# Kernel tuning notes

Hardware: AMD Instinct MI355X
Metric: run time of the kernel (lower is better)

The kernel has to match this reference:

```python
import jax, jax.numpy as jnp
import numpy as np

ALPHA = 2.0   # snntorch ATan surrogate default
THRESH = 1.0  # snntorch Leaky default threshold

@jax.custom_vjp
def spike(x):
    return (x > 0).astype(x.dtype)

def _spike_fwd(x):
    return spike(x), x

def _spike_bwd(x, g):
    # ATan surrogate gradient: (alpha/2) / (1 + (pi/2 * alpha * x)^2)
    return (g * (ALPHA / 2) / (1 + (jnp.pi / 2 * ALPHA * x) ** 2),)

spike.defvjp(_spike_fwd, _spike_bwd)

def _lif(inp, mem, beta):
    # snntorch Leaky, reset_mechanism='subtract':
    # reset from previous mem (detached), then integrate, then fire
    reset = jax.lax.stop_gradient(spike(mem - THRESH))
    mem = jnp.clip(beta, 0.0, 1.0) * mem + inp - reset * THRESH
    spk = spike(mem - THRESH)
    return spk, mem

def setup_inputs() -> dict:
    key = jax.random.key(0)
    ks = jax.random.split(key, 8)
    V, H, T, B = 32000, 512, 512, 8
    s = 0.02
    inv = 1.0 / np.sqrt(H)
    return {
        "x": jax.random.randint(ks[0], (T, B), 0, V),
        "emb": jax.random.normal(ks[1], (V, H), jnp.float32) * s,
        "pos_emb": jax.random.normal(ks[2], (T, H), jnp.float32) * s,
        "beta1": jnp.full((H,), 0.9, jnp.float32),
        "beta2": jnp.full((H,), 0.9, jnp.float32),
        "beta3": jnp.full((H,), 0.9, jnp.float32),
        "W2": jax.random.normal(ks[3], (H, H), jnp.float32) * inv,
        "b2": jnp.zeros((H,), jnp.float32),
        "W3": jax.random.normal(ks[4], (H, H), jnp.float32) * inv,
        "b3": jnp.zeros((H,), jnp.float32),
        "Wout": jax.random.normal(ks[5], (V, H), jnp.float32) * inv,
        "bout": jnp.zeros((V,), jnp.float32),
    }

def reference(x, emb, pos_emb, beta1, beta2, beta3, W2, b2, W3, b3, Wout, bout):
    T, B = x.shape
    H = emb.shape[1]
    # precompute token + positional embedding for all steps: [T, B, H]
    hid = emb[x] + pos_emb[:, None, :]
    mem0 = jnp.zeros((B, H), emb.dtype)

    def step(carry, h_t):
        m1, m2, m3 = carry
        spk1, m1 = _lif(h_t, m1, beta1)
        h = jax.nn.relu(spk1 @ W2.T + b2)
        spk2, m2 = _lif(h, m2, beta2)
        h = jax.nn.relu(spk2 @ W3.T + b3)
        spk3, m3 = _lif(h, m3, beta3)
        logits = spk3 @ Wout.T + bout  # [B, V]
        return (m1, m2, m3), logits

    _, out = jax.lax.scan(step, (mem0, mem0, mem0), hid)
    return out  # [T, B, V]
```

## Files before the change

kernel.cpp:

```cpp
#include <hip/hip_runtime.h>

#define TT 512
#define BB 8
#define HH 512
#define VV 32000
#define RR (TT * BB)

__device__ __forceinline__ float clip01(float x) { return fminf(fmaxf(x, 0.0f), 1.0f); }

__global__ void __launch_bounds__(512) snn_scan_kernel(
        const int* __restrict__ x, const float* __restrict__ emb,
        const float* __restrict__ pos,
        const float* __restrict__ beta1, const float* __restrict__ beta2,
        const float* __restrict__ beta3,
        const float* __restrict__ W2, const float* __restrict__ b2,
        const float* __restrict__ W3, const float* __restrict__ b3,
        int* __restrict__ act1, int* __restrict__ act2, int* __restrict__ act3,
        int* __restrict__ cnt3_g) {
    __shared__ int x_lds[TT];
    __shared__ int c1[TT], c2[TT], c3[TT];
    const int b = blockIdx.x;
    const int h = threadIdx.x;

    x_lds[h] = x[h * BB + b];
    c1[h] = 0; c2[h] = 0; c3[h] = 0;
    __syncthreads();

    {
        float bt = clip01(beta1[h]);
        float m = 0.0f;
        for (int t0 = 0; t0 < TT; t0 += 32) {
            float ev[32], pv[32];
#pragma unroll
            for (int u = 0; u < 32; ++u) {
                int xv = x_lds[t0 + u];
                ev[u] = emb[((size_t)xv << 9) + h];
                pv[u] = pos[((t0 + u) << 9) + h];
            }
#pragma unroll
            for (int u = 0; u < 32; ++u) {
                float inp = ev[u] + pv[u];
                float reset = (m > 1.0f) ? 1.0f : 0.0f;
                m = bt * m + inp - reset;
                if (m > 1.0f) {
                    int t = t0 + u;
                    int p = atomicAdd(&c1[t], 1);
                    act1[((t * BB + b) << 9) + p] = h;
                }
            }
        }
    }
    __syncthreads();

    {
        float bh = b2[h];
        float inp0 = fmaxf(bh, 0.0f);
        float bt = clip01(beta2[h]);
        float m = 0.0f;
        for (int t0 = 0; t0 < TT; t0 += 16) {
            int n[16];
#pragma unroll
            for (int u = 0; u < 16; ++u) n[u] = c1[t0 + u];
#pragma unroll
            for (int u = 0; u < 16; ++u) {
                float inp;
                if (n[u] == 0) {
                    inp = inp0;
                } else {
                    float acc = bh;
                    const int* a = act1 + (((t0 + u) * BB + b) << 9);
                    for (int i = 0; i < n[u]; ++i) acc += W2[(h << 9) + a[i]];
                    inp = fmaxf(acc, 0.0f);
                }
                float reset = (m > 1.0f) ? 1.0f : 0.0f;
                m = bt * m + inp - reset;
                if (m > 1.0f) {
                    int t = t0 + u;
                    int p = atomicAdd(&c2[t], 1);
                    act2[((t * BB + b) << 9) + p] = h;
                }
            }
        }
    }
    __syncthreads();

    {
        float bh = b3[h];
        float inp0 = fmaxf(bh, 0.0f);
        float bt = clip01(beta3[h]);
        float m = 0.0f;
        for (int t0 = 0; t0 < TT; t0 += 16) {
            int n[16];
#pragma unroll
            for (int u = 0; u < 16; ++u) n[u] = c2[t0 + u];
#pragma unroll
            for (int u = 0; u < 16; ++u) {
                float inp;
                if (n[u] == 0) {
                    inp = inp0;
                } else {
                    float acc = bh;
                    const int* a = act2 + (((t0 + u) * BB + b) << 9);
                    for (int i = 0; i < n[u]; ++i) acc += W3[(h << 9) + a[i]];
                    inp = fmaxf(acc, 0.0f);
                }
                float reset = (m > 1.0f) ? 1.0f : 0.0f;
                m = bt * m + inp - reset;
                if (m > 1.0f) {
                    int t = t0 + u;
                    int p = atomicAdd(&c3[t], 1);
                    act3[((t * BB + b) << 9) + p] = h;
                }
            }
        }
    }
    __syncthreads();
    cnt3_g[h * BB + b] = c3[h];
}

#define ROWS_PER_BLK 8

__global__ void __launch_bounds__(512) out_gemm_kernel(
        const int* __restrict__ cnt, const int* __restrict__ act,
        const float* __restrict__ Wout, const float* __restrict__ bout,
        float* __restrict__ out) {
    const int tid = threadIdx.x;
    const int v0 = tid * 4;

    float4 bv[16];
#pragma unroll
    for (int k = 0; k < 16; ++k) {
        int v = v0 + k * 2048;
        if (v < VV) bv[k] = *(const float4*)(bout + v);
    }

    const int r0 = blockIdx.x * ROWS_PER_BLK;
#pragma unroll
    for (int rr = 0; rr < ROWS_PER_BLK; ++rr) {
        const int r = r0 + rr;
        const int n = cnt[r];
        float* __restrict__ orow = out + (size_t)r * VV;
        if (n == 0) {
#pragma unroll
            for (int k = 0; k < 16; ++k) {
                int v = v0 + k * 2048;
                if (v < VV) *(float4*)(orow + v) = bv[k];
            }
        } else {
            const int* __restrict__ a = act + (r << 9);
#pragma unroll
            for (int k = 0; k < 16; ++k) {
                int v = v0 + k * 2048;
                if (v < VV) {
                    float4 acc = bv[k];
                    for (int i = 0; i < n; ++i) {
                        int kk = a[i];
                        acc.x += Wout[(size_t)(v + 0) * HH + kk];
                        acc.y += Wout[(size_t)(v + 1) * HH + kk];
                        acc.z += Wout[(size_t)(v + 2) * HH + kk];
                        acc.w += Wout[(size_t)(v + 3) * HH + kk];
                    }
                    *(float4*)(orow + v) = acc;
                }
            }
        }
    }
}

extern "C" void kernel_launch(void* const* d_in, const int* in_sizes, int n_in,
                              void* d_out, int out_size, void* d_ws, size_t ws_size,
                              hipStream_t stream) {
    const int*   x     = (const int*)d_in[0];
    const float* emb   = (const float*)d_in[1];
    const float* pos   = (const float*)d_in[2];
    const float* beta1 = (const float*)d_in[3];
    const float* beta2 = (const float*)d_in[4];
    const float* beta3 = (const float*)d_in[5];
    const float* W2    = (const float*)d_in[6];
    const float* b2    = (const float*)d_in[7];
    const float* W3    = (const float*)d_in[8];
    const float* b3    = (const float*)d_in[9];
    const float* Wout  = (const float*)d_in[10];
    const float* bout  = (const float*)d_in[11];
    float* out = (float*)d_out;

    int* act1 = (int*)d_ws;
    int* act2 = act1 + (size_t)RR * HH;
    int* act3 = act2 + (size_t)RR * HH;
    int* cnt3 = act3 + (size_t)RR * HH;

    snn_scan_kernel<<<BB, HH, 0, stream>>>(x, emb, pos, beta1, beta2, beta3,
                                           W2, b2, W3, b3, act1, act2, act3, cnt3);
    out_gemm_kernel<<<RR / ROWS_PER_BLK, HH, 0, stream>>>(cnt3, act3, Wout, bout, out);
}
```

Measured before the change: 687.0 us.

## Overlap bias broadcast of output rows with the serial scan kernel

Extra blocks are added to the scan launch. They write the bias vector into every output row while the eight scan blocks run the serial LIF recurrence. The second kernel becomes a fixup that leaves early when all its rows have zero spikes, and only computes sparse logits for rows that fired. This hides the 524 MB output write behind the latency-bound scan. The cost is that rows with spikes get written twice, and the extra blocks compete with the scan blocks for bandwidth.

Result: slower. 711.8 us (+3.6%).

```diff
diff --git a/kernel.cpp b/kernel.cpp
--- a/kernel.cpp
+++ b/kernel.cpp
@@ -6,9 +6,13 @@
 #define VV 32000
 #define RR (TT * BB)
 
+#define SCAN_BLOCKS  8
+#define BCAST_ROWS   8
+#define BCAST_BLOCKS (RR / BCAST_ROWS)
+
 __device__ __forceinline__ float clip01(float x) { return fminf(fmaxf(x, 0.0f), 1.0f); }
 
-__global__ void __launch_bounds__(512) snn_scan_kernel(
+__global__ void __launch_bounds__(512) scan_bcast_kernel(
         const int* __restrict__ x, const float* __restrict__ emb,
         const float* __restrict__ pos,
         const float* __restrict__ beta1, const float* __restrict__ beta2,
@@ -16,7 +20,31 @@
         const float* __restrict__ W2, const float* __restrict__ b2,
         const float* __restrict__ W3, const float* __restrict__ b3,
         int* __restrict__ act1, int* __restrict__ act2, int* __restrict__ act3,
-        int* __restrict__ cnt3_g) {
+        int* __restrict__ cnt3_g,
+        const float* __restrict__ bout, float* __restrict__ out) {
+
+    if (blockIdx.x >= SCAN_BLOCKS) {
+        const int tid = threadIdx.x;
+        const int v0 = tid * 4;
+        float4 bv[16];
+#pragma unroll
+        for (int k = 0; k < 16; ++k) {
+            int v = v0 + k * 2048;
+            if (v < VV) bv[k] = *(const float4*)(bout + v);
+        }
+        const int r0 = (blockIdx.x - SCAN_BLOCKS) * BCAST_ROWS;
+#pragma unroll
+        for (int rr = 0; rr < BCAST_ROWS; ++rr) {
+            float* __restrict__ orow = out + (size_t)(r0 + rr) * VV;
+#pragma unroll
+            for (int k = 0; k < 16; ++k) {
+                int v = v0 + k * 2048;
+                if (v < VV) *(float4*)(orow + v) = bv[k];
+            }
+        }
+        return;
+    }
+
     __shared__ int x_lds[TT];
     __shared__ int c1[TT], c2[TT], c3[TT];
     const int b = blockIdx.x;
@@ -118,50 +146,40 @@
     cnt3_g[h * BB + b] = c3[h];
 }
 
-#define ROWS_PER_BLK 8
-
-__global__ void __launch_bounds__(512) out_gemm_kernel(
+__global__ void __launch_bounds__(512) fixup_kernel(
         const int* __restrict__ cnt, const int* __restrict__ act,
         const float* __restrict__ Wout, const float* __restrict__ bout,
         float* __restrict__ out) {
+    __shared__ int ns[BCAST_ROWS];
+    const int r0 = blockIdx.x * BCAST_ROWS;
+    if (threadIdx.x < BCAST_ROWS) ns[threadIdx.x] = cnt[r0 + threadIdx.x];
+    __syncthreads();
+    int any = 0;
+#pragma unroll
+    for (int i = 0; i < BCAST_ROWS; ++i) any |= ns[i];
+    if (any == 0) return;
+
     const int tid = threadIdx.x;
     const int v0 = tid * 4;
-
-    float4 bv[16];
-#pragma unroll
-    for (int k = 0; k < 16; ++k) {
-        int v = v0 + k * 2048;
-        if (v < VV) bv[k] = *(const float4*)(bout + v);
-    }
-
-    const int r0 = blockIdx.x * ROWS_PER_BLK;
-#pragma unroll
-    for (int rr = 0; rr < ROWS_PER_BLK; ++rr) {
+    for (int rr = 0; rr < BCAST_ROWS; ++rr) {
+        const int n = ns[rr];
+        if (n == 0) continue;
         const int r = r0 + rr;
-        const int n = cnt[r];
+        const int* __restrict__ a = act + (r << 9);
         float* __restrict__ orow = out + (size_t)r * VV;
-        if (n == 0) {
-#pragma unroll
-            for (int k = 0; k < 16; ++k) {
-                int v = v0 + k * 2048;
-                if (v < VV) *(float4*)(orow + v) = bv[k];
-            }
-        } else {
-            const int* __restrict__ a = act + (r << 9);
-#pragma unroll
-            for (int k = 0; k < 16; ++k) {
-                int v = v0 + k * 2048;
-                if (v < VV) {
-                    float4 acc = bv[k];
-                    for (int i = 0; i < n; ++i) {
-                        int kk = a[i];
-                        acc.x += Wout[(size_t)(v + 0) * HH + kk];
-                        acc.y += Wout[(size_t)(v + 1) * HH + kk];
-                        acc.z += Wout[(size_t)(v + 2) * HH + kk];
-                        acc.w += Wout[(size_t)(v + 3) * HH + kk];
-                    }
-                    *(float4*)(orow + v) = acc;
-                }
+#pragma unroll
+        for (int k = 0; k < 16; ++k) {
+            int v = v0 + k * 2048;
+            if (v < VV) {
+                float4 acc = *(const float4*)(bout + v);
+                for (int i = 0; i < n; ++i) {
+                    int kk = a[i];
+                    acc.x += Wout[(size_t)(v + 0) * HH + kk];
+                    acc.y += Wout[(size_t)(v + 1) * HH + kk];
+                    acc.z += Wout[(size_t)(v + 2) * HH + kk];
+                    acc.w += Wout[(size_t)(v + 3) * HH + kk];
+                }
+                *(float4*)(orow + v) = acc;
             }
         }
     }
@@ -189,7 +207,8 @@
     int* act3 = act2 + (size_t)RR * HH;
     int* cnt3 = act3 + (size_t)RR * HH;
 
-    snn_scan_kernel<<<BB, HH, 0, stream>>>(x, emb, pos, beta1, beta2, beta3,
-                                           W2, b2, W3, b3, act1, act2, act3, cnt3);
-    out_gemm_kernel<<<RR / ROWS_PER_BLK, HH, 0, stream>>>(cnt3, act3, Wout, bout, out);
+    scan_bcast_kernel<<<SCAN_BLOCKS + BCAST_BLOCKS, HH, 0, stream>>>(
+        x, emb, pos, beta1, beta2, beta3, W2, b2, W3, b3,
+        act1, act2, act3, cnt3, bout, out);
+    fixup_kernel<<<BCAST_BLOCKS, HH, 0, stream>>>(cnt3, act3, Wout, bout, out);
 }
```
